# Optimization experiments

Measured on AMD Instinct MI355X. Metric: run time of the kernel, lower is better.

Reference implementation:

```python
import jax, jax.numpy as jnp
import numpy as np


def setup_inputs() -> dict:
    key = jax.random.key(0)
    ks = jax.random.split(key, 7)
    OUT, IN, K = 4096, 4096, 2048
    U_STORED, VT_STORED = 512, 1024  # int(0.5*(K//2+1)), int(0.5*(IN//2+1))
    return {
        "x": jax.random.normal(ks[0], (1024, IN), dtype=jnp.float32),
        "U_real": jax.random.normal(ks[1], (OUT, U_STORED), dtype=jnp.float32) * 0.01,
        "U_imag": jax.random.normal(ks[2], (OUT, U_STORED), dtype=jnp.float32) * 0.01,
        "S": jax.random.normal(ks[3], (K,), dtype=jnp.float32) * 0.02,
        "Vt_real": jax.random.normal(ks[4], (K, VT_STORED), dtype=jnp.float32) * 0.01,
        "Vt_imag": jax.random.normal(ks[5], (K, VT_STORED), dtype=jnp.float32) * 0.01,
        "bias": jnp.zeros((OUT,), dtype=jnp.float32),
    }


def _decompress(coeffs_real, coeffs_imag, n):
    # Zero-pad truncated rfft coefficients back to n//2+1, then inverse rfft.
    c = jax.lax.complex(coeffs_real, coeffs_imag)
    num_unique = n // 2 + 1
    pad = num_unique - c.shape[-1]
    if pad > 0:
        c = jnp.pad(c, ((0, 0), (0, pad)))
    elif pad < 0:
        c = c[..., :num_unique]
    return jnp.fft.irfft(c, n=n, axis=-1)


def reference(x, U_real, U_imag, S, Vt_real, Vt_imag, bias):
    k_rank = S.shape[0]
    in_features = x.shape[-1]
    U = _decompress(U_real, U_imag, k_rank)            # (out, k)
    Vh = _decompress(Vt_real, Vt_imag, in_features)    # (k, in)
    W = (U * S[None, :]) @ Vh                          # (out, in) reconstructed weight
    return x @ W.T + bias                              # F.linear(x, W, bias)
```

## Files before the change

### kernel.cpp

```cpp
#include <hip/hip_runtime.h>
#include <math.h>
#include <stdint.h>

#define PI2 6.28318530717958647692f

typedef __bf16 bf16x8 __attribute__((ext_vector_type(8)));
typedef float f32x4 __attribute__((ext_vector_type(4)));

typedef __attribute__((address_space(1))) const void gvoid_t;
typedef __attribute__((address_space(3))) void lvoid_t;

__device__ __forceinline__ void g2l16(const void* g, void* l) {
    __builtin_amdgcn_global_load_lds(
        reinterpret_cast<gvoid_t*>(reinterpret_cast<uintptr_t>(g)),
        reinterpret_cast<lvoid_t*>(reinterpret_cast<uintptr_t>(l)),
        16, 0, 0);
}

__device__ __forceinline__ short f2bf(float f) {
    unsigned u = __float_as_uint(f);
    u += 0x7FFFu + ((u >> 16) & 1u);
    return (short)(u >> 16);
}

__device__ __forceinline__ unsigned pack2bf(float a, float b) {
    return (unsigned)(unsigned short)f2bf(a) |
           ((unsigned)(unsigned short)f2bf(b) << 16);
}

__device__ __forceinline__ float bflo(unsigned v) { return __uint_as_float(v << 16); }
__device__ __forceinline__ float bfhi(unsigned v) { return __uint_as_float(v & 0xFFFF0000u); }

__device__ __forceinline__ int xcd_swizzle(int blk, int G) {
    return (blk & 7) * (G >> 3) + (blk >> 3);
}

__global__ __launch_bounds__(256) void aux_all8(
    const float* __restrict__ x,
    const float* __restrict__ Ur, const float* __restrict__ Ui,
    const float* __restrict__ S,
    const float* __restrict__ Vr, const float* __restrict__ Vi,
    short* __restrict__ xe, short* __restrict__ xo,
    short* __restrict__ B1f, short* __restrict__ VSe, short* __restrict__ VSo,
    short* __restrict__ B2, short* __restrict__ Ucat)
{
    __shared__ float tlds0[64][68];
    __shared__ float tlds1[64][68];
    __shared__ float s_lo[64], s_hi[64];
    const int b   = (int)blockIdx.x;
    const int tid = threadIdx.x;

    if (b < 1024) {
        unsigned i = (b * 256u + tid) * 8u;
        int r = i >> 11, j0 = i & 2047;
        const float* xr = x + (size_t)r * 4096 + j0;
        float4 a0 = ((const float4*)xr)[0], a1 = ((const float4*)xr)[1];
        float4 b0 = ((const float4*)(xr + 2048))[0],
               b1 = ((const float4*)(xr + 2048))[1];
        uint4 oe = {pack2bf(a0.x + b0.x, a0.y + b0.y),
                    pack2bf(a0.z + b0.z, a0.w + b0.w),
                    pack2bf(a1.x + b1.x, a1.y + b1.y),
                    pack2bf(a1.z + b1.z, a1.w + b1.w)};
        *(uint4*)(xe + i) = oe;
        uint4 oo = {pack2bf(a0.x - b0.x, a0.y - b0.y),
                    pack2bf(a0.z - b0.z, a0.w - b0.w),
                    pack2bf(a1.x - b1.x, a1.y - b1.y),
                    pack2bf(a1.z - b1.z, a1.w - b1.w)};
        *(uint4*)(xo + i) = oo;
    } else if (b < 3072) {
        unsigned i = ((b - 1024) * 256u + tid) * 8u;
        int r = i >> 11, j0 = i & 2047;
        const float inv_n = 1.0f / 4096.0f;
        float v[8];
        if (r < 512) {
            if (r == 0) {
                #pragma unroll
                for (int u = 0; u < 8; ++u) v[u] = inv_n;
            } else {
                #pragma unroll
                for (int u = 0; u < 8; ++u) {
                    int t = (r * (j0 + u)) & 2047;
                    v[u] = 2.0f * inv_n * cosf((float)t * (PI2 / 2048.0f));
                }
            }
        } else if (r < 1024) {
            int m = r - 512;
            #pragma unroll
            for (int u = 0; u < 8; ++u) {
                int t = (m * (j0 + u)) & 2047;
                v[u] = -2.0f * inv_n * sinf((float)t * (PI2 / 2048.0f));
            }
        } else if (r < 1536) {
            int c = 2 * (r - 1024) + 1;
            #pragma unroll
            for (int u = 0; u < 8; ++u) {
                int t = (c * (j0 + u)) & 4095;
                v[u] = 2.0f * inv_n * cosf((float)t * (PI2 / 4096.0f));
            }
        } else {
            int m = 2 * (r - 1536) + 1;
            #pragma unroll
            for (int u = 0; u < 8; ++u) {
                int t = (m * (j0 + u)) & 4095;
                v[u] = -2.0f * inv_n * sinf((float)t * (PI2 / 4096.0f));
            }
        }
        uint4 o = {pack2bf(v[0], v[1]), pack2bf(v[2], v[3]),
                   pack2bf(v[4], v[5]), pack2bf(v[6], v[7])};
        *(uint4*)(B1f + i) = o;
    } else if (b < 3584) {
        const int bb  = b - 3072;
        const int m   = bb >> 8;
        const int tt  = bb & 255;
        const int tkk = tt >> 4;
        const int tc  = tt & 15;
        const float* srcA = (m ? Vi : Vr) + (size_t)(tkk * 64) * 1024 + tc * 64;
        const float* srcB = srcA + (size_t)1024 * 1024;

        #pragma unroll
        for (int pass = 0; pass < 4; ++pass) {
            int r  = pass * 16 + (tid >> 4);
            int cq = (tid & 15) * 4;
            *(float4*)&tlds0[r][cq] = *(const float4*)(srcA + (size_t)r * 1024 + cq);
            *(float4*)&tlds1[r][cq] = *(const float4*)(srcB + (size_t)r * 1024 + cq);
        }
        if (tid < 64) {
            s_lo[tid] = S[tkk * 64 + tid];
            s_hi[tid] = S[tkk * 64 + tid + 1024];
        }
        __syncthreads();

        const int cl = tid & 63;
        const int ch = (tid >> 6) * 16;
        const int c  = tc * 64 + cl;
        const int f  = ((c & 1) << 10) + (m << 9) + (c >> 1);
        float ve[16], vo[16];
        #pragma unroll
        for (int j = 0; j < 16; ++j) {
            float a   = tlds0[ch + j][cl] * s_lo[ch + j];
            float bb2 = tlds1[ch + j][cl] * s_hi[ch + j];
            ve[j] = a + bb2;
            vo[j] = a - bb2;
        }
        uint4* de = (uint4*)(VSe + (size_t)f * 1024 + tkk * 64 + ch);
        de[0] = (uint4){pack2bf(ve[0],  ve[1]),  pack2bf(ve[2],  ve[3]),
                        pack2bf(ve[4],  ve[5]),  pack2bf(ve[6],  ve[7])};
        de[1] = (uint4){pack2bf(ve[8],  ve[9]),  pack2bf(ve[10], ve[11]),
                        pack2bf(ve[12], ve[13]), pack2bf(ve[14], ve[15])};
        uint4* dox = (uint4*)(VSo + (size_t)f * 1024 + tkk * 64 + ch);
        dox[0] = (uint4){pack2bf(vo[0],  vo[1]),  pack2bf(vo[2],  vo[3]),
                         pack2bf(vo[4],  vo[5]),  pack2bf(vo[6],  vo[7])};
        dox[1] = (uint4){pack2bf(vo[8],  vo[9]),  pack2bf(vo[10], vo[11]),
                         pack2bf(vo[12], vo[13]), pack2bf(vo[14], vo[15])};
    } else if (b < 4096) {
        unsigned i = ((b - 3584) * 256u + tid) * 8u;
        int p = i >> 10, k0 = i & 1023;
        int grp = p >> 8, pp = p & 255;
        const float inv_n = 1.0f / 2048.0f;
        float v[8];
        if (grp == 0) {
            if (p == 0) {
                #pragma unroll
                for (int u = 0; u < 8; ++u) v[u] = inv_n;
            } else {
                #pragma unroll
                for (int u = 0; u < 8; ++u) {
                    int t = (pp * (k0 + u)) & 1023;
                    v[u] = 2.0f * inv_n * cosf((float)t * (PI2 / 1024.0f));
                }
            }
        } else if (grp == 1) {
            #pragma unroll
            for (int u = 0; u < 8; ++u) {
                int t = (pp * (k0 + u)) & 1023;
                v[u] = -2.0f * inv_n * sinf((float)t * (PI2 / 1024.0f));
            }
        } else if (grp == 2) {
            int q = 2 * pp + 1;
            #pragma unroll
            for (int u = 0; u < 8; ++u) {
                int t = (q * (k0 + u)) & 2047;
                v[u] = 2.0f * inv_n * cosf((float)t * (PI2 / 2048.0f));
            }
        } else {
            int q = 2 * pp + 1;
            #pragma unroll
            for (int u = 0; u < 8; ++u) {
                int t = (q * (k0 + u)) & 2047;
                v[u] = -2.0f * inv_n * sinf((float)t * (PI2 / 2048.0f));
            }
        }
        uint4 o = {pack2bf(v[0], v[1]), pack2bf(v[2], v[3]),
                   pack2bf(v[4], v[5]), pack2bf(v[6], v[7])};
        *(uint4*)(B2 + i) = o;
    } else {
        unsigned i = ((b - 4096) * 256u + tid) * 8u;
        int o_ = i >> 10, c = i & 1023;
        int grp = c >> 8, cc = c & 255;
        int par = grp >> 1;
        const float2* s2 = (const float2*)(((grp & 1) ? Ui : Ur)
                                           + (size_t)o_ * 512 + 2 * cc);
        float v[8];
        #pragma unroll
        for (int j = 0; j < 8; ++j) {
            float2 q = s2[j];
            v[j] = par ? q.y : q.x;
        }
        uint4 o = {pack2bf(v[0], v[1]), pack2bf(v[2], v[3]),
                   pack2bf(v[4], v[5]), pack2bf(v[6], v[7])};
        *(uint4*)(Ucat + i) = o;
    }
}

__device__ __forceinline__ void tile_core(
    const short* __restrict__ A, int lda,
    const short* __restrict__ B, int ldb, int K,
    short* As, short* Bs, int bm, int bn, f32x4 (&acc)[4][4])
{
    const int tid  = threadIdx.x;
    const int wave = tid >> 6;
    const int lane = tid & 63;
    const int wm   = (wave >> 1) << 6;
    const int wn   = (wave & 1) << 6;
    const int l16  = lane & 15;
    const int quad = lane >> 4;
    const int rk   = l16 & 7;

    int aoff[4], boff[4], loff[4];
    #pragma unroll
    for (int p = 0; p < 4; ++p) {
        int L   = p * 256 + wave * 64 + lane;
        int row = L >> 3;
        int swz = (L & 7) ^ (row & 7);
        aoff[p] = (bm + row) * lda + swz * 8;
        boff[p] = (bn + row) * ldb + swz * 8;
        loff[p] = L * 8;
    }

    #pragma unroll
    for (int p = 0; p < 4; ++p) g2l16(A + aoff[p], As + loff[p]);
    #pragma unroll
    for (int p = 0; p < 4; ++p) g2l16(B + boff[p], Bs + loff[p]);
    __syncthreads();

    int cur = 0;
    for (int k0 = 0; k0 < K; k0 += 64) {
        const int nxt = cur ^ 1;
        if (k0 + 64 < K) {
            #pragma unroll
            for (int p = 0; p < 4; ++p)
                g2l16(A + aoff[p] + k0 + 64, As + nxt * 8192 + loff[p]);
            #pragma unroll
            for (int p = 0; p < 4; ++p)
                g2l16(B + boff[p] + k0 + 64, Bs + nxt * 8192 + loff[p]);
        }

        const short* Asc = As + cur * 8192;
        const short* Bsc = Bs + cur * 8192;
        #pragma unroll
        for (int h = 0; h < 2; ++h) {
            const int cs8 = ((((h << 2) | quad) ^ rk) << 3);
            bf16x8 b[4];
            #pragma unroll
            for (int nt = 0; nt < 4; ++nt)
                b[nt] = *(const bf16x8*)(Bsc + (wn + nt * 16 + l16) * 64 + cs8);
            #pragma unroll
            for (int mt = 0; mt < 4; ++mt) {
                bf16x8 a = *(const bf16x8*)(Asc + (wm + mt * 16 + l16) * 64 + cs8);
                #pragma unroll
                for (int nt = 0; nt < 4; ++nt)
                    acc[mt][nt] = __builtin_amdgcn_mfma_f32_16x16x32_bf16(
                        a, b[nt], acc[mt][nt], 0, 0, 0);
            }
        }
        __syncthreads();
        cur = nxt;
    }
}

__device__ __forceinline__ void store_tile_bf16(
    f32x4 (&acc)[4][4], short* __restrict__ C, int ldc, int bm, int bn)
{
    const int tid  = threadIdx.x;
    const int wave = tid >> 6;
    const int lane = tid & 63;
    const int wm   = (wave >> 1) << 6;
    const int wn   = (wave & 1) << 6;
    const int l16  = lane & 15;
    const int quad = lane >> 4;
    #pragma unroll
    for (int nt = 0; nt < 4; ++nt) {
        int col = bn + wn + nt * 16 + l16;
        #pragma unroll
        for (int mt = 0; mt < 4; ++mt) {
            int rowb = bm + wm + mt * 16 + quad * 4;
            #pragma unroll
            for (int r = 0; r < 4; ++r)
                C[(size_t)(rowb + r) * ldc + col] = f2bf(acc[mt][nt][r]);
        }
    }
}

__device__ __forceinline__ void store_frag(
    f32x4 (&acc)[4][4], short* __restrict__ planeTile)
{
    uint4* p = (uint4*)planeTile;
    const int tid = threadIdx.x;
    #pragma unroll
    for (int c = 0; c < 8; ++c) {
        int nt = c >> 1, mt0 = (c & 1) * 2;
        uint4 o = {pack2bf(acc[mt0][nt][0],     acc[mt0][nt][1]),
                   pack2bf(acc[mt0][nt][2],     acc[mt0][nt][3]),
                   pack2bf(acc[mt0 + 1][nt][0], acc[mt0 + 1][nt][1]),
                   pack2bf(acc[mt0 + 1][nt][2], acc[mt0 + 1][nt][3])};
        p[c * 256 + tid] = o;
    }
}

template <bool OUT_F32>
__device__ __forceinline__ void reduce_unit(
    const short* __restrict__ P, size_t planeU4, int SK,
    int tile, int c, int tilesX, void* __restrict__ Out, int ldc,
    const float* __restrict__ bias)
{
    const int bm = (tile / tilesX) << 7;
    const int bn = (tile % tilesX) << 7;
    const int tid  = threadIdx.x;
    const int wave = tid >> 6;
    const int lane = tid & 63;
    const int wm   = (wave >> 1) << 6;
    const int wn   = (wave & 1) << 6;
    const int l16  = lane & 15;
    const int quad = lane >> 4;
    const int nt   = c >> 1, mt0 = (c & 1) * 2;

    const uint4* P4 = (const uint4*)P;
    const size_t base = (size_t)tile * 2048 + (size_t)c * 256 + tid;
    float f[8] = {0, 0, 0, 0, 0, 0, 0, 0};
    for (int z = 0; z < SK; ++z) {
        uint4 v = P4[(size_t)z * planeU4 + base];
        f[0] += bflo(v.x); f[1] += bfhi(v.x);
        f[2] += bflo(v.y); f[3] += bfhi(v.y);
        f[4] += bflo(v.z); f[5] += bfhi(v.z);
        f[6] += bflo(v.w); f[7] += bfhi(v.w);
    }
    const int col = bn + wn + nt * 16 + l16;
    float bv = 0.f;
    if (OUT_F32) bv = bias[col];
    #pragma unroll
    for (int j = 0; j < 8; ++j) {
        int mt  = mt0 + (j >> 2);
        int row = bm + wm + mt * 16 + quad * 4 + (j & 3);
        if (OUT_F32)
            ((float*)Out)[(size_t)row * ldc + col] = f[j] + bv;
        else
            ((short*)Out)[(size_t)row * ldc + col] = f2bf(f[j]);
    }
}

__global__ __launch_bounds__(256, 2) void gemm_s1w2(
    const short* __restrict__ xe, const short* __restrict__ xo,
    const short* __restrict__ B1f,
    const short* __restrict__ B2,
    const short* __restrict__ VSe, const short* __restrict__ VSo,
    short* __restrict__ P, short* __restrict__ PW)
{
    __shared__ __align__(16) short As[2 * 128 * 64];
    __shared__ __align__(16) short Bs[2 * 128 * 64];

    f32x4 acc[4][4];
    #pragma unroll
    for (int i = 0; i < 4; ++i)
        #pragma unroll
        for (int j = 0; j < 4; ++j)
            acc[i][j] = (f32x4){0.f, 0.f, 0.f, 0.f};

    const int raw = (int)blockIdx.x;
    if (raw < 512) {
        const int u    = xcd_swizzle(raw, 512);
        const int z    = u >> 7;
        const int tile = u & 127;
        const int tx   = tile & 15, ty = tile >> 4;
        const bool odd = (tx & 8) != 0;
        const short* A = (odd ? xo : xe) + (size_t)z * 512;
        const short* B = B1f + (odd ? (size_t)1024 * 2048 : 0) + (size_t)z * 512;
        const int bm   = ty << 7;
        const int bn   = (tx & 7) << 7;

        tile_core(A, 2048, B, 2048, 512, As, Bs, bm, bn, acc);
        store_frag(acc, P + (size_t)z * 2097152 + (size_t)tile * 16384);
    } else {
        const int u    = xcd_swizzle(raw - 512, 512);
        const int z    = u >> 7;
        const int tile = u & 127;
        const int bm   = (tile >> 4) << 7;
        const int bn   = (tile & 15) << 7;
        const short* Bv = (bm < 512) ? VSe : VSo;

        tile_core(B2 + (size_t)z * 256, 1024, Bv + (size_t)z * 256, 1024,
                  256, As, Bs, bm, bn, acc);
        store_frag(acc, PW + (size_t)z * 2097152 + (size_t)tile * 16384);
    }
}

__global__ __launch_bounds__(256) void reduce_s1w2(
    const short* __restrict__ P, const short* __restrict__ PW,
    short* __restrict__ Xp, short* __restrict__ W2)
{
    const int b   = (int)blockIdx.x;
    const int sub = b & 1023;
    if (b < 1024)
        reduce_unit<false>(P,  (size_t)2097152 >> 3, 4, sub >> 3, sub & 7,
                           16, Xp, 2048, nullptr);
    else
        reduce_unit<false>(PW, (size_t)2097152 >> 3, 4, sub >> 3, sub & 7,
                           16, W2, 2048, nullptr);
}

__global__ __launch_bounds__(256, 2) void gemm_sk_frag(
    const short* __restrict__ A, int lda,
    const short* __restrict__ B, int ldb,
    short* __restrict__ P, size_t planeShorts, int Kpart,
    int tileShift, int tilesXShift)
{
    __shared__ __align__(16) short As[2 * 128 * 64];
    __shared__ __align__(16) short Bs[2 * 128 * 64];

    f32x4 acc[4][4];
    #pragma unroll
    for (int i = 0; i < 4; ++i)
        #pragma unroll
        for (int j = 0; j < 4; ++j)
            acc[i][j] = (f32x4){0.f, 0.f, 0.f, 0.f};

    const int u    = xcd_swizzle((int)blockIdx.x, (int)gridDim.x);
    const int z    = u >> tileShift;
    const int tile = u & ((1 << tileShift) - 1);
    const int bm   = (tile >> tilesXShift) << 7;
    const int bn   = (tile & ((1 << tilesXShift) - 1)) << 7;

    tile_core(A + (size_t)z * Kpart, lda, B + (size_t)z * Kpart, ldb, Kpart,
              As, Bs, bm, bn, acc);
    store_frag(acc, P + (size_t)z * planeShorts + (size_t)tile * 16384);
}

template <bool OUT_F32>
__global__ __launch_bounds__(256) void reduce_frag(
    const short* __restrict__ P, size_t planeShorts, int SK,
    int tilesX, void* __restrict__ Out, int ldc,
    const float* __restrict__ bias)
{
    reduce_unit<OUT_F32>(P, planeShorts >> 3, SK,
                         (int)(blockIdx.x >> 3), (int)(blockIdx.x & 7),
                         tilesX, Out, ldc, bias);
}

template <bool OUT_F32>
__global__ __launch_bounds__(256, 2) void gemm_direct(
    const short* __restrict__ A, int lda,
    const short* __restrict__ B, int ldb,
    void* __restrict__ Cv, int ldc,
    const float* __restrict__ bias, int K)
{
    __shared__ __align__(16) short As[2 * 128 * 64];
    __shared__ __align__(16) short Bs[2 * 128 * 64];

    f32x4 acc[4][4];
    #pragma unroll
    for (int i = 0; i < 4; ++i)
        #pragma unroll
        for (int j = 0; j < 4; ++j)
            acc[i][j] = (f32x4){0.f, 0.f, 0.f, 0.f};

    const int bm = blockIdx.y << 7;
    const int bn = blockIdx.x << 7;
    tile_core(A, lda, B, ldb, K, As, Bs, bm, bn, acc);

    const int tid  = threadIdx.x;
    const int wave = tid >> 6;
    const int lane = tid & 63;
    const int wm   = (wave >> 1) << 6;
    const int wn   = (wave & 1) << 6;
    const int l16  = lane & 15;
    const int quad = lane >> 4;

    if (OUT_F32) {
        float* C = (float*)Cv;
        #pragma unroll
        for (int nt = 0; nt < 4; ++nt) {
            int col = bn + wn + nt * 16 + l16;
            float bv = bias ? bias[col] : 0.f;
            #pragma unroll
            for (int mt = 0; mt < 4; ++mt) {
                int rowb = bm + wm + mt * 16 + quad * 4;
                #pragma unroll
                for (int r = 0; r < 4; ++r)
                    C[(size_t)(rowb + r) * ldc + col] = acc[mt][nt][r] + bv;
            }
        }
    } else {
        store_tile_bf16(acc, (short*)Cv, ldc, bm, bn);
    }
}

__global__ __launch_bounds__(256, 2) void gemm_s1f_dir(
    const short* __restrict__ xe, const short* __restrict__ xo,
    const short* __restrict__ B1f, short* __restrict__ Xp)
{
    __shared__ __align__(16) short As[2 * 128 * 64];
    __shared__ __align__(16) short Bs[2 * 128 * 64];

    f32x4 acc[4][4];
    #pragma unroll
    for (int i = 0; i < 4; ++i)
        #pragma unroll
        for (int j = 0; j < 4; ++j)
            acc[i][j] = (f32x4){0.f, 0.f, 0.f, 0.f};

    const int u    = (int)blockIdx.x;
    const int tx   = u & 15, ty = u >> 4;
    const bool odd = (tx & 8) != 0;
    const short* A = odd ? xo : xe;
    const short* B = B1f + (odd ? (size_t)1024 * 2048 : 0);
    const int bm   = ty << 7;
    const int bn   = (tx & 7) << 7;

    tile_core(A, 2048, B, 2048, 2048, As, Bs, bm, bn, acc);
    store_tile_bf16(acc, Xp, 2048, bm, bn + (odd ? 1024 : 0));
}

extern "C" void kernel_launch(void* const* d_in, const int* in_sizes, int n_in,
                              void* d_out, int out_size, void* d_ws, size_t ws_size,
                              hipStream_t stream) {
    const float* x    = (const float*)d_in[0];
    const float* Ur   = (const float*)d_in[1];
    const float* Ui   = (const float*)d_in[2];
    const float* S    = (const float*)d_in[3];
    const float* Vr   = (const float*)d_in[4];
    const float* Vi   = (const float*)d_in[5];
    const float* bias = (const float*)d_in[6];
    float* out = (float*)d_out;

    short* ws    = (short*)d_ws;
    short* xe    = ws;
    short* xo    = xe    + (size_t)1024 * 2048;
    short* B1f   = xo    + (size_t)1024 * 2048;
    short* VSe   = B1f   + (size_t)2048 * 2048;
    short* VSo   = VSe   + (size_t)2048 * 1024;
    short* B2    = VSo   + (size_t)2048 * 1024;
    short* Ucat  = B2    + (size_t)1024 * 1024;
    short* Xp    = Ucat  + (size_t)4096 * 1024;
    short* W2    = Xp    + (size_t)1024 * 2048;
    short* Gm    = W2    + (size_t)1024 * 2048;
    short* Pp    = Gm    + (size_t)1024 * 1024;
    short* PW    = Pp    + (size_t)8388608;

    const size_t need = (size_t)((char*)(PW + (size_t)8388608) - (char*)d_ws);

    aux_all8<<<dim3(6144), 256, 0, stream>>>(
        x, Ur, Ui, S, Vr, Vi, xe, xo, B1f, VSe, VSo, B2, Ucat);

    if (ws_size >= need) {
        gemm_s1w2<<<dim3(1024), 256, 0, stream>>>(
            xe, xo, B1f, B2, VSe, VSo, Pp, PW);
        reduce_s1w2<<<dim3(2048), 256, 0, stream>>>(Pp, PW, Xp, W2);

        gemm_sk_frag<<<dim3(512), 256, 0, stream>>>(
            Xp, 2048, W2, 2048, Pp, (size_t)1048576, 256, 6, 3);
        reduce_frag<false><<<dim3(512), 256, 0, stream>>>(
            Pp, (size_t)1048576, 8, 8, Gm, 1024, nullptr);

        gemm_direct<true><<<dim3(32, 8), 256, 0, stream>>>(
            Gm, 1024, Ucat, 1024, out, 4096, bias, 1024);
    } else {
        gemm_s1f_dir<<<dim3(128), 256, 0, stream>>>(xe, xo, B1f, Xp);
        gemm_direct<false><<<dim3(16, 4), 256, 0, stream>>>(
            B2, 1024, VSe, 1024, W2, 2048, nullptr, 1024);
        gemm_direct<false><<<dim3(16, 4), 256, 0, stream>>>(
            B2 + (size_t)512 * 1024, 1024, VSo, 1024,
            W2 + (size_t)512 * 2048, 2048, nullptr, 1024);
        gemm_direct<false><<<dim3(8, 8), 256, 0, stream>>>(
            Xp, 2048, W2, 2048, Gm, 1024, nullptr, 2048);
        gemm_direct<true><<<dim3(32, 8), 256, 0, stream>>>(
            Gm, 1024, Ucat, 1024, out, 4096, bias, 1024);
    }
}
```

Measured before the change: 164.4 us.

## Apply a second radix-2 even/odd split to the input-side inverse DFT GEMM

Splits the even-frequency half of the input-side inverse real DFT once more (xee/xeo with a 1024-long basis B1e), so that half of the first GEMM stage works with K=256 per split instead of 512. The VS row permutation is updated to match the new output ordering, and the fallback path replaces the dedicated kernel with three gemm_direct calls. This removes about a quarter of the stage-1 MACs and shrinks the basis tables. In exchange, the preprocessing does more adds and the tiles become imbalanced, since even tiles now run a shorter K loop than odd tiles.

After: 159.8 us. 2.8% less time.

```diff
diff --git a/kernel.cpp b/kernel.cpp
--- a/kernel.cpp
+++ b/kernel.cpp
@@ -40,8 +40,9 @@
     const float* __restrict__ Ur, const float* __restrict__ Ui,
     const float* __restrict__ S,
     const float* __restrict__ Vr, const float* __restrict__ Vi,
-    short* __restrict__ xe, short* __restrict__ xo,
-    short* __restrict__ B1f, short* __restrict__ VSe, short* __restrict__ VSo,
+    short* __restrict__ xee, short* __restrict__ xeo, short* __restrict__ xo,
+    short* __restrict__ B1e, short* __restrict__ B1o,
+    short* __restrict__ VSe, short* __restrict__ VSo,
     short* __restrict__ B2, short* __restrict__ Ucat)
 {
     __shared__ float tlds0[64][68];
@@ -50,55 +51,95 @@
     const int b   = (int)blockIdx.x;
     const int tid = threadIdx.x;
 
-    if (b < 1024) {
+    if (b < 512) {
         unsigned i = (b * 256u + tid) * 8u;
-        int r = i >> 11, j0 = i & 2047;
+        int r = i >> 10, j0 = i & 1023;
         const float* xr = x + (size_t)r * 4096 + j0;
-        float4 a0 = ((const float4*)xr)[0], a1 = ((const float4*)xr)[1];
-        float4 b0 = ((const float4*)(xr + 2048))[0],
-               b1 = ((const float4*)(xr + 2048))[1];
-        uint4 oe = {pack2bf(a0.x + b0.x, a0.y + b0.y),
-                    pack2bf(a0.z + b0.z, a0.w + b0.w),
-                    pack2bf(a1.x + b1.x, a1.y + b1.y),
-                    pack2bf(a1.z + b1.z, a1.w + b1.w)};
-        *(uint4*)(xe + i) = oe;
-        uint4 oo = {pack2bf(a0.x - b0.x, a0.y - b0.y),
-                    pack2bf(a0.z - b0.z, a0.w - b0.w),
-                    pack2bf(a1.x - b1.x, a1.y - b1.y),
-                    pack2bf(a1.z - b1.z, a1.w - b1.w)};
-        *(uint4*)(xo + i) = oo;
-    } else if (b < 3072) {
-        unsigned i = ((b - 1024) * 256u + tid) * 8u;
-        int r = i >> 11, j0 = i & 2047;
+        float4 p0 = ((const float4*)xr)[0],        p1 = ((const float4*)xr)[1];
+        float4 q0 = ((const float4*)(xr + 1024))[0], q1 = ((const float4*)(xr + 1024))[1];
+        float4 s0 = ((const float4*)(xr + 2048))[0], s1 = ((const float4*)(xr + 2048))[1];
+        float4 t0 = ((const float4*)(xr + 3072))[0], t1 = ((const float4*)(xr + 3072))[1];
+        float el[8] = {p0.x + s0.x, p0.y + s0.y, p0.z + s0.z, p0.w + s0.w,
+                       p1.x + s1.x, p1.y + s1.y, p1.z + s1.z, p1.w + s1.w};
+        float eh[8] = {q0.x + t0.x, q0.y + t0.y, q0.z + t0.z, q0.w + t0.w,
+                       q1.x + t1.x, q1.y + t1.y, q1.z + t1.z, q1.w + t1.w};
+        float ol[8] = {p0.x - s0.x, p0.y - s0.y, p0.z - s0.z, p0.w - s0.w,
+                       p1.x - s1.x, p1.y - s1.y, p1.z - s1.z, p1.w - s1.w};
+        float oh[8] = {q0.x - t0.x, q0.y - t0.y, q0.z - t0.z, q0.w - t0.w,
+                       q1.x - t1.x, q1.y - t1.y, q1.z - t1.z, q1.w - t1.w};
+        size_t base1k = (size_t)r * 1024 + j0;
+        uint4 oee = {pack2bf(el[0] + eh[0], el[1] + eh[1]),
+                     pack2bf(el[2] + eh[2], el[3] + eh[3]),
+                     pack2bf(el[4] + eh[4], el[5] + eh[5]),
+                     pack2bf(el[6] + eh[6], el[7] + eh[7])};
+        *(uint4*)(xee + base1k) = oee;
+        uint4 oeo = {pack2bf(el[0] - eh[0], el[1] - eh[1]),
+                     pack2bf(el[2] - eh[2], el[3] - eh[3]),
+                     pack2bf(el[4] - eh[4], el[5] - eh[5]),
+                     pack2bf(el[6] - eh[6], el[7] - eh[7])};
+        *(uint4*)(xeo + base1k) = oeo;
+        size_t base2k = (size_t)r * 2048 + j0;
+        uint4 olo = {pack2bf(ol[0], ol[1]), pack2bf(ol[2], ol[3]),
+                     pack2bf(ol[4], ol[5]), pack2bf(ol[6], ol[7])};
+        *(uint4*)(xo + base2k) = olo;
+        uint4 ohi = {pack2bf(oh[0], oh[1]), pack2bf(oh[2], oh[3]),
+                     pack2bf(oh[4], oh[5]), pack2bf(oh[6], oh[7])};
+        *(uint4*)(xo + base2k + 1024) = ohi;
+    } else if (b < 1024) {
+        unsigned i = ((b - 512) * 256u + tid) * 8u;
+        int p = i >> 10, j0 = i & 1023;
         const float inv_n = 1.0f / 4096.0f;
         float v[8];
-        if (r < 512) {
-            if (r == 0) {
+        if (p < 256) {
+            if (p == 0) {
                 #pragma unroll
                 for (int u = 0; u < 8; ++u) v[u] = inv_n;
             } else {
                 #pragma unroll
                 for (int u = 0; u < 8; ++u) {
-                    int t = (r * (j0 + u)) & 2047;
-                    v[u] = 2.0f * inv_n * cosf((float)t * (PI2 / 2048.0f));
+                    int t = (p * (j0 + u)) & 1023;
+                    v[u] = 2.0f * inv_n * cosf((float)t * (PI2 / 1024.0f));
                 }
             }
-        } else if (r < 1024) {
-            int m = r - 512;
-            #pragma unroll
-            for (int u = 0; u < 8; ++u) {
-                int t = (m * (j0 + u)) & 2047;
+        } else if (p < 512) {
+            int a = p - 256;
+            #pragma unroll
+            for (int u = 0; u < 8; ++u) {
+                int t = (a * (j0 + u)) & 1023;
+                v[u] = -2.0f * inv_n * sinf((float)t * (PI2 / 1024.0f));
+            }
+        } else if (p < 768) {
+            int q = 2 * (p - 512) + 1;
+            #pragma unroll
+            for (int u = 0; u < 8; ++u) {
+                int t = (q * (j0 + u)) & 2047;
+                v[u] = 2.0f * inv_n * cosf((float)t * (PI2 / 2048.0f));
+            }
+        } else {
+            int q = 2 * (p - 768) + 1;
+            #pragma unroll
+            for (int u = 0; u < 8; ++u) {
+                int t = (q * (j0 + u)) & 2047;
                 v[u] = -2.0f * inv_n * sinf((float)t * (PI2 / 2048.0f));
             }
-        } else if (r < 1536) {
-            int c = 2 * (r - 1024) + 1;
+        }
+        uint4 o = {pack2bf(v[0], v[1]), pack2bf(v[2], v[3]),
+                   pack2bf(v[4], v[5]), pack2bf(v[6], v[7])};
+        *(uint4*)(B1e + i) = o;
+    } else if (b < 2048) {
+        unsigned i = ((b - 1024) * 256u + tid) * 8u;
+        int p = i >> 11, j0 = i & 2047;
+        const float inv_n = 1.0f / 4096.0f;
+        float v[8];
+        if (p < 512) {
+            int c = 2 * p + 1;
             #pragma unroll
             for (int u = 0; u < 8; ++u) {
                 int t = (c * (j0 + u)) & 4095;
                 v[u] = 2.0f * inv_n * cosf((float)t * (PI2 / 4096.0f));
             }
         } else {
-            int m = 2 * (r - 1536) + 1;
+            int m = 2 * (p - 512) + 1;
             #pragma unroll
             for (int u = 0; u < 8; ++u) {
                 int t = (m * (j0 + u)) & 4095;
@@ -107,9 +148,9 @@
         }
         uint4 o = {pack2bf(v[0], v[1]), pack2bf(v[2], v[3]),
                    pack2bf(v[4], v[5]), pack2bf(v[6], v[7])};
-        *(uint4*)(B1f + i) = o;
-    } else if (b < 3584) {
-        const int bb  = b - 3072;
+        *(uint4*)(B1o + i) = o;
+    } else if (b < 2560) {
+        const int bb  = b - 2048;
         const int m   = bb >> 8;
         const int tt  = bb & 255;
         const int tkk = tt >> 4;
@@ -133,7 +174,13 @@
         const int cl = tid & 63;
         const int ch = (tid >> 6) * 16;
         const int c  = tc * 64 + cl;
-        const int f  = ((c & 1) << 10) + (m << 9) + (c >> 1);
+        int f;
+        if (c & 1) {
+            f = 1024 + (m << 9) + (c >> 1);
+        } else {
+            int r2 = c >> 1;
+            f = ((r2 & 1) << 9) + (m << 8) + (r2 >> 1);
+        }
         float ve[16], vo[16];
         #pragma unroll
         for (int j = 0; j < 16; ++j) {
@@ -152,8 +199,8 @@
                          pack2bf(vo[4],  vo[5]),  pack2bf(vo[6],  vo[7])};
         dox[1] = (uint4){pack2bf(vo[8],  vo[9]),  pack2bf(vo[10], vo[11]),
                          pack2bf(vo[12], vo[13]), pack2bf(vo[14], vo[15])};
-    } else if (b < 4096) {
-        unsigned i = ((b - 3584) * 256u + tid) * 8u;
+    } else if (b < 3072) {
+        unsigned i = ((b - 2560) * 256u + tid) * 8u;
         int p = i >> 10, k0 = i & 1023;
         int grp = p >> 8, pp = p & 255;
         const float inv_n = 1.0f / 2048.0f;
@@ -194,7 +241,7 @@
                    pack2bf(v[4], v[5]), pack2bf(v[6], v[7])};
         *(uint4*)(B2 + i) = o;
     } else {
-        unsigned i = ((b - 4096) * 256u + tid) * 8u;
+        unsigned i = ((b - 3072) * 256u + tid) * 8u;
         int o_ = i >> 10, c = i & 1023;
         int grp = c >> 8, cc = c & 255;
         int par = grp >> 1;
@@ -359,8 +406,9 @@
 }
 
 __global__ __launch_bounds__(256, 2) void gemm_s1w2(
-    const short* __restrict__ xe, const short* __restrict__ xo,
-    const short* __restrict__ B1f,
+    const short* __restrict__ xee, const short* __restrict__ xeo,
+    const short* __restrict__ xo,
+    const short* __restrict__ B1e, const short* __restrict__ B1o,
     const short* __restrict__ B2,
     const short* __restrict__ VSe, const short* __restrict__ VSo,
     short* __restrict__ P, short* __restrict__ PW)
@@ -381,13 +429,16 @@
         const int z    = u >> 7;
         const int tile = u & 127;
         const int tx   = tile & 15, ty = tile >> 4;
-        const bool odd = (tx & 8) != 0;
-        const short* A = (odd ? xo : xe) + (size_t)z * 512;
-        const short* B = B1f + (odd ? (size_t)1024 * 2048 : 0) + (size_t)z * 512;
         const int bm   = ty << 7;
-        const int bn   = (tx & 7) << 7;
-
-        tile_core(A, 2048, B, 2048, 512, As, Bs, bm, bn, acc);
+        if (tx < 8) {
+            const short* A = ((tx & 4) ? xeo : xee) + (size_t)z * 256;
+            const short* B = B1e + (size_t)z * 256;
+            tile_core(A, 1024, B, 1024, 256, As, Bs, bm, tx << 7, acc);
+        } else {
+            const short* A = xo + (size_t)z * 512;
+            const short* B = B1o + (size_t)z * 512;
+            tile_core(A, 2048, B, 2048, 512, As, Bs, bm, (tx & 7) << 7, acc);
+        }
         store_frag(acc, P + (size_t)z * 2097152 + (size_t)tile * 16384);
     } else {
         const int u    = xcd_swizzle(raw - 512, 512);
@@ -501,32 +552,6 @@
     } else {
         store_tile_bf16(acc, (short*)Cv, ldc, bm, bn);
     }
-}
-
-__global__ __launch_bounds__(256, 2) void gemm_s1f_dir(
-    const short* __restrict__ xe, const short* __restrict__ xo,
-    const short* __restrict__ B1f, short* __restrict__ Xp)
-{
-    __shared__ __align__(16) short As[2 * 128 * 64];
-    __shared__ __align__(16) short Bs[2 * 128 * 64];
-
-    f32x4 acc[4][4];
-    #pragma unroll
-    for (int i = 0; i < 4; ++i)
-        #pragma unroll
-        for (int j = 0; j < 4; ++j)
-            acc[i][j] = (f32x4){0.f, 0.f, 0.f, 0.f};
-
-    const int u    = (int)blockIdx.x;
-    const int tx   = u & 15, ty = u >> 4;
-    const bool odd = (tx & 8) != 0;
-    const short* A = odd ? xo : xe;
-    const short* B = B1f + (odd ? (size_t)1024 * 2048 : 0);
-    const int bm   = ty << 7;
-    const int bn   = (tx & 7) << 7;
-
-    tile_core(A, 2048, B, 2048, 2048, As, Bs, bm, bn, acc);
-    store_tile_bf16(acc, Xp, 2048, bm, bn + (odd ? 1024 : 0));
 }
 
 extern "C" void kernel_launch(void* const* d_in, const int* in_sizes, int n_in,
@@ -542,10 +567,12 @@
     float* out = (float*)d_out;
 
     short* ws    = (short*)d_ws;
-    short* xe    = ws;
-    short* xo    = xe    + (size_t)1024 * 2048;
-    short* B1f   = xo    + (size_t)1024 * 2048;
-    short* VSe   = B1f   + (size_t)2048 * 2048;
+    short* xee   = ws;
+    short* xeo   = xee   + (size_t)1024 * 1024;
+    short* xo    = xeo   + (size_t)1024 * 1024;
+    short* B1e   = xo    + (size_t)1024 * 2048;
+    short* B1o   = B1e   + (size_t)1024 * 1024;
+    short* VSe   = B1o   + (size_t)1024 * 2048;
     short* VSo   = VSe   + (size_t)2048 * 1024;
     short* B2    = VSo   + (size_t)2048 * 1024;
     short* Ucat  = B2    + (size_t)1024 * 1024;
@@ -557,12 +584,12 @@
 
     const size_t need = (size_t)((char*)(PW + (size_t)8388608) - (char*)d_ws);
 
-    aux_all8<<<dim3(6144), 256, 0, stream>>>(
-        x, Ur, Ui, S, Vr, Vi, xe, xo, B1f, VSe, VSo, B2, Ucat);
+    aux_all8<<<dim3(5120), 256, 0, stream>>>(
+        x, Ur, Ui, S, Vr, Vi, xee, xeo, xo, B1e, B1o, VSe, VSo, B2, Ucat);
 
     if (ws_size >= need) {
         gemm_s1w2<<<dim3(1024), 256, 0, stream>>>(
-            xe, xo, B1f, B2, VSe, VSo, Pp, PW);
+            xee, xeo, xo, B1e, B1o, B2, VSe, VSo, Pp, PW);
         reduce_s1w2<<<dim3(2048), 256, 0, stream>>>(Pp, PW, Xp, W2);
 
         gemm_sk_frag<<<dim3(512), 256, 0, stream>>>(
@@ -573,7 +600,13 @@
         gemm_direct<true><<<dim3(32, 8), 256, 0, stream>>>(
             Gm, 1024, Ucat, 1024, out, 4096, bias, 1024);
     } else {
-        gemm_s1f_dir<<<dim3(128), 256, 0, stream>>>(xe, xo, B1f, Xp);
+        gemm_direct<false><<<dim3(4, 8), 256, 0, stream>>>(
+            xee, 1024, B1e, 1024, Xp, 2048, nullptr, 1024);
+        gemm_direct<false><<<dim3(4, 8), 256, 0, stream>>>(
+            xeo, 1024, B1e + (size_t)512 * 1024, 1024, Xp + 512, 2048,
+            nullptr, 1024);
+        gemm_direct<false><<<dim3(8, 8), 256, 0, stream>>>(
+            xo, 2048, B1o, 2048, Xp + 1024, 2048, nullptr, 2048);
         gemm_direct<false><<<dim3(16, 4), 256, 0, stream>>>(
             B2, 1024, VSe, 1024, W2, 2048, nullptr, 1024);
         gemm_direct<false><<<dim3(16, 4), 256, 0, stream>>>(
```
